# Performance work log

Measured on AMD Instinct MI355X. Metric: run time of the kernel, lower is better.

## Reference

```python
import jax, jax.numpy as jnp
import numpy as np

N_NODES = 50000
N_EDGES = 800000
IN_F = 128
OUT_F = 128
N_LAYERS = 2


def setup_inputs() -> dict:
    key = jax.random.key(0)
    ks = jax.random.split(key, 8)
    x = jax.random.normal(ks[0], (N_NODES, IN_F), dtype=jnp.float32)
    hidden_states = jax.random.normal(ks[1], (N_LAYERS, N_NODES, OUT_F), dtype=jnp.float32)
    src = jax.random.randint(ks[2], (N_EDGES,), 0, N_NODES)
    dst = jax.random.randint(ks[3], (N_EDGES,), 0, N_NODES)
    edge_w = jax.random.uniform(ks[4], (N_EDGES,), dtype=jnp.float32)
    # [layer, gate(r,u,c), in+out, out], scaled like typical init
    W_self = jax.random.normal(ks[5], (N_LAYERS, 3, IN_F + OUT_F, OUT_F), dtype=jnp.float32) * 0.05
    W_neigh = jax.random.normal(ks[6], (N_LAYERS, 3, IN_F + OUT_F, OUT_F), dtype=jnp.float32) * 0.05
    bias = jax.random.uniform(ks[7], (N_LAYERS, 3, OUT_F), dtype=jnp.float32)
    return {"x": x, "hidden_states": hidden_states, "src": src, "dst": dst,
            "edge_w": edge_w, "W_self": W_self, "W_neigh": W_neigh, "bias": bias}


def _gconv(z, src, dst, edge_w, ws, wn):
    # z: [N, 2F]; message passing: sum_{e: dst=v} edge_w[e] * z[src[e]]
    msg = z[src] * edge_w[:, None]                      # [E, 2F]
    agg = jax.ops.segment_sum(msg, dst, num_segments=N_NODES)  # [N, 2F]
    return z @ ws + agg @ wn                            # [N, F]


def _cell(x, h, src, dst, edge_w, ws, wn, b):
    # ws/wn: [3, 2F, F], b: [3, F]; gates r,u,c as in GraphGRUCell
    xh = jnp.concatenate([x, h], axis=1)
    r = jax.nn.sigmoid(_gconv(xh, src, dst, edge_w, ws[0], wn[0]) + b[0])
    u = jax.nn.sigmoid(_gconv(xh, src, dst, edge_w, ws[1], wn[1]) + b[1])
    xh2 = jnp.concatenate([x, r * h], axis=1)
    c = jax.nn.sigmoid(_gconv(xh2, src, dst, edge_w, ws[2], wn[2]) + b[2])
    return u * h + (1.0 - u) * c


def reference(x, hidden_states, src, dst, edge_w, W_self, W_neigh, bias):
    hiddens = []
    for i in range(N_LAYERS):  # small fixed layer count
        x = _cell(x, hidden_states[i], src, dst, edge_w, W_self[i], W_neigh[i], bias[i])
        hiddens.append(x)
    return (x, hiddens)
```

## Files before the change

kernel.cpp:

```cpp
#include <hip/hip_runtime.h>
#include <math.h>

#define F 128
#define NLAYERS 2

typedef __attribute__((ext_vector_type(8))) short bf16x8s;
typedef __attribute__((ext_vector_type(8))) unsigned short u16x8;
typedef __attribute__((ext_vector_type(4))) float f32x4;

__device__ __forceinline__ float sigmoidf_(float x) { return 1.0f / (1.0f + expf(-x)); }

__device__ __forceinline__ unsigned short f2bf(float f) {
    unsigned int u = __float_as_uint(f);
    u += 0x7fffu + ((u >> 16) & 1u);
    return (unsigned short)(u >> 16);
}
__device__ __forceinline__ float bf2f(unsigned short s) {
    return __uint_as_float(((unsigned int)s) << 16);
}

__global__ void pack_w_bf16(const float* __restrict__ Ws, const float* __restrict__ Wn,
                            unsigned short* __restrict__ W1b, unsigned short* __restrict__ W2b) {
    int t = blockIdx.x * blockDim.x + threadIdx.x;
    const int n1 = 2 * 64 * 256 * 8;
    if (t < n1) {
        int j = t & 7, n = (t >> 3) & 255, ko = (t >> 11) & 63, l = t >> 17;
        int k = ko * 8 + j;
        int p = k >> 7, r = k & 127, g = n >> 7, c = n & 127;
        const float* W = (p < 2) ? Ws : Wn;
        W1b[t] = f2bf(W[(((l * 3 + g) * 256) + ((p & 1) * 128 + r)) * 128 + c]);
    } else {
        int t2 = t - n1;
        if (t2 >= 2 * 64 * 128 * 8) return;
        int j = t2 & 7, n = (t2 >> 3) & 127, ko = (t2 >> 10) & 63, l = t2 >> 16;
        int k = ko * 8 + j;
        int p = k >> 7, r = k & 127;
        const float* W = (p < 2) ? Ws : Wn;
        W2b[t2] = f2bf(W[(((l * 3 + 2) * 256) + ((p & 1) * 128 + r)) * 128 + n]);
    }
}

__global__ void cvt_bf16_i(const float* __restrict__ in, unsigned short* __restrict__ out, int n4) {
    int t = blockIdx.x * blockDim.x + threadIdx.x;
    if (t >= n4) return;
    float4 v = reinterpret_cast<const float4*>(in)[t];
    ushort4 o;
    o.x = f2bf(v.x); o.y = f2bf(v.y); o.z = f2bf(v.z); o.w = f2bf(v.w);
    *reinterpret_cast<ushort4*>(out + (((size_t)(t >> 5)) << 8) + ((t & 31) << 2)) = o;
}

__global__ void hist_dst(const int* __restrict__ dst, int* __restrict__ cnt, int E) {
    int e = blockIdx.x * blockDim.x + threadIdx.x;
    if (e < E) atomicAdd(&cnt[dst[e]], 1);
}

__global__ __launch_bounds__(1024) void scan_blk(const int* __restrict__ cnt,
                                                 int* __restrict__ offs,
                                                 int* __restrict__ bsum, int n) {
    __shared__ int wsum[16];
    int tid = threadIdx.x, lane = tid & 63, wid = tid >> 6;
    int i = blockIdx.x * 1024 + tid;
    int v = (i < n) ? cnt[i] : 0;
    int incl = v;
#pragma unroll
    for (int off = 1; off < 64; off <<= 1) {
        int t = __shfl_up(incl, off, 64);
        if (lane >= off) incl += t;
    }
    if (lane == 63) wsum[wid] = incl;
    __syncthreads();
    if (wid == 0) {
        int s = (lane < 16) ? wsum[lane] : 0;
#pragma unroll
        for (int off = 1; off < 16; off <<= 1) {
            int t = __shfl_up(s, off, 64);
            if (lane >= off) s += t;
        }
        if (lane < 16) wsum[lane] = s;
    }
    __syncthreads();
    int wbase = (wid > 0) ? wsum[wid - 1] : 0;
    if (i < n) offs[i] = wbase + incl - v;
    if (tid == 1023) bsum[blockIdx.x] = wbase + incl;
}

__global__ __launch_bounds__(1024) void scan_tops(int* __restrict__ bsum, int nb,
                                                  int* __restrict__ total_out) {
    __shared__ int wsum[16];
    int tid = threadIdx.x, lane = tid & 63, wid = tid >> 6;
    int v = (tid < nb) ? bsum[tid] : 0;
    int incl = v;
#pragma unroll
    for (int off = 1; off < 64; off <<= 1) {
        int t = __shfl_up(incl, off, 64);
        if (lane >= off) incl += t;
    }
    if (lane == 63) wsum[wid] = incl;
    __syncthreads();
    if (wid == 0) {
        int s = (lane < 16) ? wsum[lane] : 0;
#pragma unroll
        for (int off = 1; off < 16; off <<= 1) {
            int t = __shfl_up(s, off, 64);
            if (lane >= off) s += t;
        }
        if (lane < 16) wsum[lane] = s;
    }
    __syncthreads();
    int wbase = (wid > 0) ? wsum[wid - 1] : 0;
    if (tid < nb) bsum[tid] = wbase + incl - v;
    if (tid == 1023) *total_out = wbase + incl;
}

__global__ __launch_bounds__(1024) void scan_add(const int* __restrict__ bsum,
                                                 int* __restrict__ offs,
                                                 int* __restrict__ cursor, int n) {
    int i = blockIdx.x * 1024 + threadIdx.x;
    if (i >= n) return;
    int o = offs[i] + bsum[blockIdx.x];
    offs[i] = o;
    cursor[i] = o;
}

__global__ void scatter_edges(const int* __restrict__ src, const int* __restrict__ dst,
                              const float* __restrict__ ew, int* __restrict__ cursor,
                              int2* __restrict__ es, int E) {
    int e = blockIdx.x * blockDim.x + threadIdx.x;
    if (e >= E) return;
    int d = dst[e];
    int p = atomicAdd(&cursor[d], 1);
    es[p] = make_int2(src[e], __float_as_int(ew[e]));
}

__global__ __launch_bounds__(256) void agg_csr2_i(
    const unsigned short* __restrict__ XH,
    const int2* __restrict__ es, const int* __restrict__ offs,
    unsigned short* __restrict__ agg0, unsigned short* __restrict__ agg1, int N) {
    int node = blockIdx.x * 8 + (threadIdx.x >> 5);
    if (node >= N) return;
    int lane = threadIdx.x & 31;
    int beg = offs[node], end = offs[node + 1];
    float a0[8] = {0, 0, 0, 0, 0, 0, 0, 0};
    float a1[8] = {0, 0, 0, 0, 0, 0, 0, 0};
    int loff = lane << 3;
    int i = beg;
    for (; i + 3 < end; i += 4) {
        int2 e0 = es[i], e1 = es[i + 1], e2 = es[i + 2], e3 = es[i + 3];
        u16x8 v0 = *reinterpret_cast<const u16x8*>(XH + (((size_t)e0.x) << 8) + loff);
        u16x8 v1 = *reinterpret_cast<const u16x8*>(XH + (((size_t)e1.x) << 8) + loff);
        u16x8 v2 = *reinterpret_cast<const u16x8*>(XH + (((size_t)e2.x) << 8) + loff);
        u16x8 v3 = *reinterpret_cast<const u16x8*>(XH + (((size_t)e3.x) << 8) + loff);
        float w0 = __int_as_float(e0.y), w1 = __int_as_float(e1.y);
        float w2 = __int_as_float(e2.y), w3 = __int_as_float(e3.y);
#pragma unroll
        for (int j = 0; j < 8; ++j) {
            a0[j] += w0 * bf2f(v0[j]);
            a1[j] += w1 * bf2f(v1[j]);
            a0[j] += w2 * bf2f(v2[j]);
            a1[j] += w3 * bf2f(v3[j]);
        }
    }
    for (; i < end; ++i) {
        int2 e0 = es[i];
        float w0 = __int_as_float(e0.y);
        u16x8 v0 = *reinterpret_cast<const u16x8*>(XH + (((size_t)e0.x) << 8) + loff);
#pragma unroll
        for (int j = 0; j < 8; ++j) a0[j] += w0 * bf2f(v0[j]);
    }
    u16x8 o;
#pragma unroll
    for (int j = 0; j < 8; ++j) o[j] = f2bf(a0[j] + a1[j]);
    unsigned short* op = (lane < 16)
        ? (agg0 + (((size_t)node) << 7) + (lane << 3))
        : (agg1 + (((size_t)node) << 7) + ((lane & 15) << 3));
    *reinterpret_cast<u16x8*>(op) = o;
}

__global__ __launch_bounds__(256) void agg_csr1_b(
    const unsigned short* __restrict__ V0,
    const int2* __restrict__ es, const int* __restrict__ offs,
    unsigned short* __restrict__ agg0, int N) {
    int node = blockIdx.x * 8 + (threadIdx.x >> 5);
    if (node >= N) return;
    int lane = threadIdx.x & 31;
    int beg = offs[node], end = offs[node + 1];
    float p0[4] = {0, 0, 0, 0}, p1[4] = {0, 0, 0, 0};
    int loff = lane << 2;
    int i = beg;
    for (; i + 3 < end; i += 4) {
        int2 e0 = es[i], e1 = es[i + 1], e2 = es[i + 2], e3 = es[i + 3];
        ushort4 x0 = *reinterpret_cast<const ushort4*>(V0 + (((size_t)e0.x) << 7) + loff);
        ushort4 x1 = *reinterpret_cast<const ushort4*>(V0 + (((size_t)e1.x) << 7) + loff);
        ushort4 x2 = *reinterpret_cast<const ushort4*>(V0 + (((size_t)e2.x) << 7) + loff);
        ushort4 x3 = *reinterpret_cast<const ushort4*>(V0 + (((size_t)e3.x) << 7) + loff);
        float w0 = __int_as_float(e0.y), w1 = __int_as_float(e1.y);
        float w2 = __int_as_float(e2.y), w3 = __int_as_float(e3.y);
        p0[0] += w0 * bf2f(x0.x); p0[1] += w0 * bf2f(x0.y);
        p0[2] += w0 * bf2f(x0.z); p0[3] += w0 * bf2f(x0.w);
        p1[0] += w1 * bf2f(x1.x); p1[1] += w1 * bf2f(x1.y);
        p1[2] += w1 * bf2f(x1.z); p1[3] += w1 * bf2f(x1.w);
        p0[0] += w2 * bf2f(x2.x); p0[1] += w2 * bf2f(x2.y);
        p0[2] += w2 * bf2f(x2.z); p0[3] += w2 * bf2f(x2.w);
        p1[0] += w3 * bf2f(x3.x); p1[1] += w3 * bf2f(x3.y);
        p1[2] += w3 * bf2f(x3.z); p1[3] += w3 * bf2f(x3.w);
    }
    for (; i < end; ++i) {
        int2 e0 = es[i];
        float w0 = __int_as_float(e0.y);
        ushort4 x0 = *reinterpret_cast<const ushort4*>(V0 + (((size_t)e0.x) << 7) + loff);
        p0[0] += w0 * bf2f(x0.x); p0[1] += w0 * bf2f(x0.y);
        p0[2] += w0 * bf2f(x0.z); p0[3] += w0 * bf2f(x0.w);
    }
    size_t ob = (((size_t)node) << 7) + loff;
    ushort4 o0;
    o0.x = f2bf(p0[0] + p1[0]); o0.y = f2bf(p0[1] + p1[1]);
    o0.z = f2bf(p0[2] + p1[2]); o0.w = f2bf(p0[3] + p1[3]);
    *reinterpret_cast<ushort4*>(agg0 + ob) = o0;
}

__global__ __launch_bounds__(256) void gemm_mfma(
    const unsigned short* __restrict__ A0, const unsigned short* __restrict__ A1,
    const unsigned short* __restrict__ A2, const unsigned short* __restrict__ A3,
    int sA0, int sA1, int obsh,
    const unsigned short* __restrict__ Wb, const float* __restrict__ bias,
    const float* __restrict__ hfull, const float* __restrict__ uin,
    unsigned short* __restrict__ outb, float* __restrict__ outf,
    float* __restrict__ outf2, int Nn, int Ntot, int mode) {
    __shared__ __align__(16) unsigned short Als[2][4 * 64 * 8];
    __shared__ __align__(16) unsigned short Bls[2][4 * 128 * 8];
    const unsigned short* parts[4] = {A0, A1, A2, A3};

    int tid = threadIdx.x;
    int row0 = blockIdx.x * 64;
    int n0c = blockIdx.y * 128;
    int lane = tid & 63;
    int w = tid >> 6;
    int wrow = (w & 1) << 5;
    int wcol = (w >> 1) << 6;
    int quad = lane >> 4, l16 = lane & 15;

    f32x4 acc[2][4];
    const f32x4 z4 = {0.f, 0.f, 0.f, 0.f};
#pragma unroll
    for (int mt = 0; mt < 2; ++mt)
#pragma unroll
        for (int nt = 0; nt < 4; ++nt) acc[mt][nt] = z4;

    int growA = row0 + lane;
    if (growA >= Nn) growA = Nn - 1;
    int qB = tid >> 7, nB = tid & 127;

    auto stage = [&](int ks, int buf) {
        int p = ks >> 7;
        size_t roff = (p == 0) ? (size_t)growA * (size_t)sA0
                    : (p == 1) ? (size_t)growA * (size_t)sA1
                               : ((size_t)growA << 7);
        const unsigned short* ga = parts[p] + roff + (ks & 127) + (w << 3);
        __builtin_amdgcn_global_load_lds(
            (const __attribute__((address_space(1))) void*)ga,
            (__attribute__((address_space(3))) void*)&Als[buf][((w << 6) + lane) << 3], 16, 0, 0);
#pragma unroll
        for (int r = 0; r < 2; ++r) {
            int q = 2 * r + qB;
            int koG = (ks >> 3) + q;
            const unsigned short* gb = Wb + ((size_t)(koG * Ntot + n0c + nB) << 3);
            __builtin_amdgcn_global_load_lds(
                (const __attribute__((address_space(1))) void*)gb,
                (__attribute__((address_space(3))) void*)&Bls[buf][((q << 7) + nB) << 3], 16, 0, 0);
        }
    };

    stage(0, 0);
    __syncthreads();
    int buf = 0;
    for (int ks = 0; ks < 512; ks += 32, buf ^= 1) {
        if (ks + 32 < 512) stage(ks + 32, buf ^ 1);

        bf16x8s af[2], bfr[4];
#pragma unroll
        for (int mt = 0; mt < 2; ++mt)
            af[mt] = *reinterpret_cast<const bf16x8s*>(
                &Als[buf][((quad << 6) + wrow + (mt << 4) + l16) << 3]);
#pragma unroll
        for (int nt = 0; nt < 4; ++nt)
            bfr[nt] = *reinterpret_cast<const bf16x8s*>(
                &Bls[buf][((quad << 7) + wcol + (nt << 4) + l16) << 3]);
#pragma unroll
        for (int mt = 0; mt < 2; ++mt)
#pragma unroll
            for (int nt = 0; nt < 4; ++nt)
                acc[mt][nt] = __builtin_amdgcn_mfma_f32_16x16x32_bf16(
                    af[mt], bfr[nt], acc[mt][nt], 0, 0, 0);
        __syncthreads();
    }

#pragma unroll
    for (int mt = 0; mt < 2; ++mt) {
#pragma unroll
        for (int reg = 0; reg < 4; ++reg) {
            int row = row0 + wrow + (mt << 4) + (quad << 2) + reg;
            if (row >= Nn) continue;
#pragma unroll
            for (int nt = 0; nt < 4; ++nt) {
                int col = n0c + wcol + (nt << 4) + l16;
                float val = acc[mt][nt][reg] + bias[col];
                if (mode == 0) {
                    float sg = sigmoidf_(val);
                    int c = col & 127;
                    size_t o = ((size_t)row << 7) + c;
                    if (col < 128)
                        outb[o] = f2bf(sg * hfull[o]);
                    else
                        outf[o] = sg;
                } else {
                    float cv = sigmoidf_(val);
                    size_t o = ((size_t)row << 7) + col;
                    float uu = uin[o];
                    float hh = hfull[o];
                    float hn = uu * hh + (1.0f - uu) * cv;
                    outf[o] = hn;
                    if (outf2) outf2[o] = hn;
                    outb[((size_t)row << obsh) + col] = f2bf(hn);
                }
            }
        }
    }
}

extern "C" void kernel_launch(void* const* d_in, const int* in_sizes, int n_in,
                              void* d_out, int out_size, void* d_ws, size_t ws_size,
                              hipStream_t stream) {
    const float* x      = (const float*)d_in[0];
    const float* hidden = (const float*)d_in[1];
    const int*   src    = (const int*)d_in[2];
    const int*   dst    = (const int*)d_in[3];
    const float* ew     = (const float*)d_in[4];
    const float* Wself  = (const float*)d_in[5];
    const float* Wneigh = (const float*)d_in[6];
    const float* bias   = (const float*)d_in[7];
    float* out = (float*)d_out;

    int N = in_sizes[0] / F;
    int E = in_sizes[2];
    size_t NF = (size_t)N * F;

    char* p = (char*)d_ws;
    auto alloc = [&](size_t bytes) { char* r = p; p += (bytes + 255) & ~255ull; return r; };
    unsigned short* xh0    = (unsigned short*)alloc(2 * NF * 2);
    unsigned short* xh1    = (unsigned short*)alloc(2 * NF * 2);
    unsigned short* agg_xb = (unsigned short*)alloc(NF * 2);
    unsigned short* agg_hb = (unsigned short*)alloc(NF * 2);
    unsigned short* agg_rb = (unsigned short*)alloc(NF * 2);
    unsigned short* rhb    = (unsigned short*)alloc(NF * 2);
    float*          u      = (float*)alloc(NF * 4);
    unsigned short* W1b    = (unsigned short*)alloc(2 * 64 * 256 * 8 * 2);
    unsigned short* W2b    = (unsigned short*)alloc(2 * 64 * 128 * 8 * 2);
    int2*           es     = (int2*)alloc((size_t)E * 8);
    int*            cnt    = (int*)alloc((size_t)N * 4);
    int*            offs   = (int*)alloc(((size_t)N + 1) * 4);
    int*            cursor = (int*)alloc((size_t)N * 4);
    int*            bsum   = (int*)alloc(1024 * 4);

    pack_w_bf16<<<dim3(1536), dim3(256), 0, stream>>>(Wself, Wneigh, W1b, W2b);
    int n4 = (int)(NF / 4);
    int cblk = (n4 + 255) / 256;
    cvt_bf16_i<<<dim3(cblk), dim3(256), 0, stream>>>(x, xh0, n4);
    cvt_bf16_i<<<dim3(cblk), dim3(256), 0, stream>>>(hidden, xh0 + 128, n4);
    cvt_bf16_i<<<dim3(cblk), dim3(256), 0, stream>>>(hidden + NF, xh1 + 128, n4);

    hipMemsetAsync(cnt, 0, (size_t)N * sizeof(int), stream);
    int eBlocks = (E + 255) / 256;
    hist_dst<<<dim3(eBlocks), dim3(256), 0, stream>>>(dst, cnt, E);
    int nb = (N + 1023) / 1024;
    scan_blk<<<dim3(nb), dim3(1024), 0, stream>>>(cnt, offs, bsum, N);
    scan_tops<<<dim3(1), dim3(1024), 0, stream>>>(bsum, nb, offs + N);
    scan_add<<<dim3(nb), dim3(1024), 0, stream>>>(bsum, offs, cursor, N);
    scatter_edges<<<dim3(eBlocks), dim3(256), 0, stream>>>(src, dst, ew, cursor, es, E);

    float* out_x  = out;
    float* out_h1 = out + NF;
    float* out_h2 = out + 2 * NF;

    int aggBlocks = (N + 7) / 8;
    int mBlocks = (N + 63) / 64;
    for (int l = 0; l < NLAYERS; ++l) {
        unsigned short* xhL = (l == 0) ? xh0 : xh1;
        const float* hL = hidden + (size_t)l * NF;
        const float* biasL = bias + (size_t)l * 384;

        agg_csr2_i<<<dim3(aggBlocks), dim3(256), 0, stream>>>(xhL, es, offs,
                                                              agg_xb, agg_hb, N);

        gemm_mfma<<<dim3(mBlocks, 2), dim3(256), 0, stream>>>(
            xhL, xhL + 128, agg_xb, agg_hb, 256, 256, 7,
            W1b + (size_t)l * 64 * 256 * 8, biasL, hL, nullptr,
            rhb, u, nullptr, N, 256, 0);

        agg_csr1_b<<<dim3(aggBlocks), dim3(256), 0, stream>>>(rhb, es, offs, agg_rb, N);

        float* o1 = (l == 0) ? out_h1 : out_h2;
        float* o2 = (l == NLAYERS - 1) ? out_x : nullptr;
        unsigned short* obN = (l == 0) ? xh1 : agg_rb;
        int obsh = (l == 0) ? 8 : 7;
        gemm_mfma<<<dim3(mBlocks, 1), dim3(256), 0, stream>>>(
            xhL, rhb, agg_xb, agg_rb, 256, 128, obsh,
            W2b + (size_t)l * 64 * 128 * 8, biasL + 256, hL, u,
            obN, o1, o2, N, 128, 1);
    }
}
```

Baseline: 608.5 us.

## Fuse neighbor aggregation into MFMA gate GEMMs and merge conversion kernels

Fuses the CSR gather-aggregation into the r/u and c GEMM kernels, so the aggregated tile lives in swizzled shared memory instead of being written to and re-read from global memory. The r/u GEMM now covers all 256 output columns in one block instead of splitting across two blocks. The three bf16 conversion launches are merged into one. In exchange, each fused block runs a serial gather phase before its GEMM, with large LDS use that may lower occupancy and limit overlap of gather latency with MFMA work.

New measurement: 715.1 us. 17.5% more time.

```diff
diff --git a/kernel.cpp b/kernel.cpp
--- a/kernel.cpp
+++ b/kernel.cpp
@@ -40,13 +40,21 @@
     }
 }
 
-__global__ void cvt_bf16_i(const float* __restrict__ in, unsigned short* __restrict__ out, int n4) {
+__global__ void cvt_all(const float* __restrict__ x, const float* __restrict__ hidden,
+                        unsigned short* __restrict__ xh0, unsigned short* __restrict__ xh1,
+                        int n4, size_t NF) {
     int t = blockIdx.x * blockDim.x + threadIdx.x;
-    if (t >= n4) return;
-    float4 v = reinterpret_cast<const float4*>(in)[t];
+    const float* in;
+    unsigned short* out;
+    int tt;
+    if (t < n4) { in = x; out = xh0; tt = t; }
+    else if (t < 2 * n4) { in = hidden; out = xh0 + 128; tt = t - n4; }
+    else if (t < 3 * n4) { in = hidden + NF; out = xh1 + 128; tt = t - 2 * n4; }
+    else return;
+    float4 v = reinterpret_cast<const float4*>(in)[tt];
     ushort4 o;
     o.x = f2bf(v.x); o.y = f2bf(v.y); o.z = f2bf(v.z); o.w = f2bf(v.w);
-    *reinterpret_cast<ushort4*>(out + (((size_t)(t >> 5)) << 8) + ((t & 31) << 2)) = o;
+    *reinterpret_cast<ushort4*>(out + (((size_t)(tt >> 5)) << 8) + ((tt & 31) << 2)) = o;
 }
 
 __global__ void hist_dst(const int* __restrict__ dst, int* __restrict__ cnt, int E) {
@@ -132,112 +140,245 @@
     es[p] = make_int2(src[e], __float_as_int(ew[e]));
 }
 
-__global__ __launch_bounds__(256) void agg_csr2_i(
+__global__ __launch_bounds__(256) void fused_ru(
     const unsigned short* __restrict__ XH,
     const int2* __restrict__ es, const int* __restrict__ offs,
-    unsigned short* __restrict__ agg0, unsigned short* __restrict__ agg1, int N) {
-    int node = blockIdx.x * 8 + (threadIdx.x >> 5);
-    if (node >= N) return;
-    int lane = threadIdx.x & 31;
-    int beg = offs[node], end = offs[node + 1];
-    float a0[8] = {0, 0, 0, 0, 0, 0, 0, 0};
-    float a1[8] = {0, 0, 0, 0, 0, 0, 0, 0};
-    int loff = lane << 3;
-    int i = beg;
-    for (; i + 3 < end; i += 4) {
-        int2 e0 = es[i], e1 = es[i + 1], e2 = es[i + 2], e3 = es[i + 3];
-        u16x8 v0 = *reinterpret_cast<const u16x8*>(XH + (((size_t)e0.x) << 8) + loff);
-        u16x8 v1 = *reinterpret_cast<const u16x8*>(XH + (((size_t)e1.x) << 8) + loff);
-        u16x8 v2 = *reinterpret_cast<const u16x8*>(XH + (((size_t)e2.x) << 8) + loff);
-        u16x8 v3 = *reinterpret_cast<const u16x8*>(XH + (((size_t)e3.x) << 8) + loff);
-        float w0 = __int_as_float(e0.y), w1 = __int_as_float(e1.y);
-        float w2 = __int_as_float(e2.y), w3 = __int_as_float(e3.y);
-#pragma unroll
-        for (int j = 0; j < 8; ++j) {
-            a0[j] += w0 * bf2f(v0[j]);
-            a1[j] += w1 * bf2f(v1[j]);
-            a0[j] += w2 * bf2f(v2[j]);
-            a1[j] += w3 * bf2f(v3[j]);
-        }
-    }
-    for (; i < end; ++i) {
-        int2 e0 = es[i];
-        float w0 = __int_as_float(e0.y);
-        u16x8 v0 = *reinterpret_cast<const u16x8*>(XH + (((size_t)e0.x) << 8) + loff);
-#pragma unroll
-        for (int j = 0; j < 8; ++j) a0[j] += w0 * bf2f(v0[j]);
-    }
-    u16x8 o;
-#pragma unroll
-    for (int j = 0; j < 8; ++j) o[j] = f2bf(a0[j] + a1[j]);
-    unsigned short* op = (lane < 16)
-        ? (agg0 + (((size_t)node) << 7) + (lane << 3))
-        : (agg1 + (((size_t)node) << 7) + ((lane & 15) << 3));
-    *reinterpret_cast<u16x8*>(op) = o;
-}
-
-__global__ __launch_bounds__(256) void agg_csr1_b(
-    const unsigned short* __restrict__ V0,
+    const unsigned short* __restrict__ Wb, const float* __restrict__ bias,
+    const float* __restrict__ hfull,
+    unsigned short* __restrict__ aggx_out,
+    unsigned short* __restrict__ rhb, float* __restrict__ u, int N) {
+    __shared__ __align__(16) unsigned short AGG[64 * 256];
+    __shared__ __align__(16) unsigned short Als[2][4 * 64 * 8];
+    __shared__ __align__(16) unsigned short Bls[2][4 * 256 * 8];
+
+    int tid = threadIdx.x;
+    int row0 = blockIdx.x * 64;
+    int lane64 = tid & 63, w = tid >> 6;
+    int lane32 = tid & 31, grp = tid >> 5;
+
+    int growA = row0 + lane64;
+    if (growA >= N) growA = N - 1;
+
+    {
+        const unsigned short* ga = XH + (size_t)growA * 256 + (w << 3);
+        __builtin_amdgcn_global_load_lds(
+            (const __attribute__((address_space(1))) void*)ga,
+            (__attribute__((address_space(3))) void*)&Als[0][((w << 6) + lane64) << 3], 16, 0, 0);
+#pragma unroll
+        for (int r = 0; r < 4; ++r) {
+            int idx = (r << 8) + tid;
+            int q = idx >> 8, n = idx & 255;
+            const unsigned short* gb = Wb + ((size_t)(q * 256 + n) << 3);
+            __builtin_amdgcn_global_load_lds(
+                (const __attribute__((address_space(1))) void*)gb,
+                (__attribute__((address_space(3))) void*)&Bls[0][((q << 8) + n) << 3], 16, 0, 0);
+        }
+    }
+
+    int loff = lane32 << 3;
+    for (int ln = grp; ln < 64; ln += 8) {
+        int node = row0 + ln;
+        float a0[8] = {0, 0, 0, 0, 0, 0, 0, 0};
+        float a1[8] = {0, 0, 0, 0, 0, 0, 0, 0};
+        if (node < N) {
+            int beg = offs[node], end = offs[node + 1];
+            int i = beg;
+            for (; i + 3 < end; i += 4) {
+                int2 e0 = es[i], e1 = es[i + 1], e2 = es[i + 2], e3 = es[i + 3];
+                u16x8 v0 = *reinterpret_cast<const u16x8*>(XH + (((size_t)e0.x) << 8) + loff);
+                u16x8 v1 = *reinterpret_cast<const u16x8*>(XH + (((size_t)e1.x) << 8) + loff);
+                u16x8 v2 = *reinterpret_cast<const u16x8*>(XH + (((size_t)e2.x) << 8) + loff);
+                u16x8 v3 = *reinterpret_cast<const u16x8*>(XH + (((size_t)e3.x) << 8) + loff);
+                float w0 = __int_as_float(e0.y), w1 = __int_as_float(e1.y);
+                float w2 = __int_as_float(e2.y), w3 = __int_as_float(e3.y);
+#pragma unroll
+                for (int j = 0; j < 8; ++j) {
+                    a0[j] += w0 * bf2f(v0[j]);
+                    a1[j] += w1 * bf2f(v1[j]);
+                    a0[j] += w2 * bf2f(v2[j]);
+                    a1[j] += w3 * bf2f(v3[j]);
+                }
+            }
+            for (; i < end; ++i) {
+                int2 e0 = es[i];
+                float w0 = __int_as_float(e0.y);
+                u16x8 v0 = *reinterpret_cast<const u16x8*>(XH + (((size_t)e0.x) << 8) + loff);
+#pragma unroll
+                for (int j = 0; j < 8; ++j) a0[j] += w0 * bf2f(v0[j]);
+            }
+        }
+        u16x8 o;
+#pragma unroll
+        for (int j = 0; j < 8; ++j) o[j] = f2bf(a0[j] + a1[j]);
+        int sidx = ln * 256 + ((lane32 << 3) ^ ((ln & 7) << 3));
+        *reinterpret_cast<u16x8*>(&AGG[sidx]) = o;
+        if (node < N && lane32 < 16)
+            *reinterpret_cast<u16x8*>(aggx_out + (((size_t)node) << 7) + (lane32 << 3)) = o;
+    }
+    __syncthreads();
+
+    int wrow = (w & 1) << 5;
+    int wcol = (w >> 1) << 7;
+    int quad = lane64 >> 4, l16 = lane64 & 15;
+
+    f32x4 acc[2][8];
+    const f32x4 z4 = {0.f, 0.f, 0.f, 0.f};
+#pragma unroll
+    for (int mt = 0; mt < 2; ++mt)
+#pragma unroll
+        for (int nt = 0; nt < 8; ++nt) acc[mt][nt] = z4;
+
+    int buf = 0;
+    for (int ks = 0; ks < 512; ks += 32, buf ^= 1) {
+        int nk = ks + 32;
+        if (nk < 512) {
+#pragma unroll
+            for (int r = 0; r < 4; ++r) {
+                int idx = (r << 8) + tid;
+                int q = idx >> 8, n = idx & 255;
+                int koG = (nk >> 3) + q;
+                const unsigned short* gb = Wb + ((size_t)(koG * 256 + n) << 3);
+                __builtin_amdgcn_global_load_lds(
+                    (const __attribute__((address_space(1))) void*)gb,
+                    (__attribute__((address_space(3))) void*)&Bls[buf ^ 1][((q << 8) + n) << 3], 16, 0, 0);
+            }
+            if (nk < 256) {
+                const unsigned short* ga = XH + (size_t)growA * 256 + nk + (w << 3);
+                __builtin_amdgcn_global_load_lds(
+                    (const __attribute__((address_space(1))) void*)ga,
+                    (__attribute__((address_space(3))) void*)&Als[buf ^ 1][((w << 6) + lane64) << 3], 16, 0, 0);
+            }
+        }
+
+        bf16x8s af[2], bfr[8];
+        if (ks < 256) {
+#pragma unroll
+            for (int mt = 0; mt < 2; ++mt)
+                af[mt] = *reinterpret_cast<const bf16x8s*>(
+                    &Als[buf][((quad << 6) + wrow + (mt << 4) + l16) << 3]);
+        } else {
+            int colk = (ks - 256) + (quad << 3);
+#pragma unroll
+            for (int mt = 0; mt < 2; ++mt) {
+                int row = wrow + (mt << 4) + l16;
+                af[mt] = *reinterpret_cast<const bf16x8s*>(
+                    &AGG[row * 256 + (colk ^ ((row & 7) << 3))]);
+            }
+        }
+#pragma unroll
+        for (int nt = 0; nt < 8; ++nt)
+            bfr[nt] = *reinterpret_cast<const bf16x8s*>(
+                &Bls[buf][((quad << 8) + wcol + (nt << 4) + l16) << 3]);
+#pragma unroll
+        for (int mt = 0; mt < 2; ++mt)
+#pragma unroll
+            for (int nt = 0; nt < 8; ++nt)
+                acc[mt][nt] = __builtin_amdgcn_mfma_f32_16x16x32_bf16(
+                    af[mt], bfr[nt], acc[mt][nt], 0, 0, 0);
+        __syncthreads();
+    }
+
+#pragma unroll
+    for (int mt = 0; mt < 2; ++mt) {
+#pragma unroll
+        for (int reg = 0; reg < 4; ++reg) {
+            int row = row0 + wrow + (mt << 4) + (quad << 2) + reg;
+            if (row >= N) continue;
+#pragma unroll
+            for (int nt = 0; nt < 8; ++nt) {
+                int col = wcol + (nt << 4) + l16;
+                float val = acc[mt][nt][reg] + bias[col];
+                float sg = sigmoidf_(val);
+                int c = col & 127;
+                size_t o = ((size_t)row << 7) + c;
+                if (col < 128)
+                    rhb[o] = f2bf(sg * hfull[o]);
+                else
+                    u[o] = sg;
+            }
+        }
+    }
+}
+
+__global__ __launch_bounds__(256) void fused_c(
+    const unsigned short* __restrict__ XH, const unsigned short* __restrict__ RHB,
+    const unsigned short* __restrict__ AGGX,
     const int2* __restrict__ es, const int* __restrict__ offs,
-    unsigned short* __restrict__ agg0, int N) {
-    int node = blockIdx.x * 8 + (threadIdx.x >> 5);
-    if (node >= N) return;
-    int lane = threadIdx.x & 31;
-    int beg = offs[node], end = offs[node + 1];
-    float p0[4] = {0, 0, 0, 0}, p1[4] = {0, 0, 0, 0};
-    int loff = lane << 2;
-    int i = beg;
-    for (; i + 3 < end; i += 4) {
-        int2 e0 = es[i], e1 = es[i + 1], e2 = es[i + 2], e3 = es[i + 3];
-        ushort4 x0 = *reinterpret_cast<const ushort4*>(V0 + (((size_t)e0.x) << 7) + loff);
-        ushort4 x1 = *reinterpret_cast<const ushort4*>(V0 + (((size_t)e1.x) << 7) + loff);
-        ushort4 x2 = *reinterpret_cast<const ushort4*>(V0 + (((size_t)e2.x) << 7) + loff);
-        ushort4 x3 = *reinterpret_cast<const ushort4*>(V0 + (((size_t)e3.x) << 7) + loff);
-        float w0 = __int_as_float(e0.y), w1 = __int_as_float(e1.y);
-        float w2 = __int_as_float(e2.y), w3 = __int_as_float(e3.y);
-        p0[0] += w0 * bf2f(x0.x); p0[1] += w0 * bf2f(x0.y);
-        p0[2] += w0 * bf2f(x0.z); p0[3] += w0 * bf2f(x0.w);
-        p1[0] += w1 * bf2f(x1.x); p1[1] += w1 * bf2f(x1.y);
-        p1[2] += w1 * bf2f(x1.z); p1[3] += w1 * bf2f(x1.w);
-        p0[0] += w2 * bf2f(x2.x); p0[1] += w2 * bf2f(x2.y);
-        p0[2] += w2 * bf2f(x2.z); p0[3] += w2 * bf2f(x2.w);
-        p1[0] += w3 * bf2f(x3.x); p1[1] += w3 * bf2f(x3.y);
-        p1[2] += w3 * bf2f(x3.z); p1[3] += w3 * bf2f(x3.w);
-    }
-    for (; i < end; ++i) {
-        int2 e0 = es[i];
-        float w0 = __int_as_float(e0.y);
-        ushort4 x0 = *reinterpret_cast<const ushort4*>(V0 + (((size_t)e0.x) << 7) + loff);
-        p0[0] += w0 * bf2f(x0.x); p0[1] += w0 * bf2f(x0.y);
-        p0[2] += w0 * bf2f(x0.z); p0[3] += w0 * bf2f(x0.w);
-    }
-    size_t ob = (((size_t)node) << 7) + loff;
-    ushort4 o0;
-    o0.x = f2bf(p0[0] + p1[0]); o0.y = f2bf(p0[1] + p1[1]);
-    o0.z = f2bf(p0[2] + p1[2]); o0.w = f2bf(p0[3] + p1[3]);
-    *reinterpret_cast<ushort4*>(agg0 + ob) = o0;
-}
-
-__global__ __launch_bounds__(256) void gemm_mfma(
-    const unsigned short* __restrict__ A0, const unsigned short* __restrict__ A1,
-    const unsigned short* __restrict__ A2, const unsigned short* __restrict__ A3,
-    int sA0, int sA1, int obsh,
     const unsigned short* __restrict__ Wb, const float* __restrict__ bias,
     const float* __restrict__ hfull, const float* __restrict__ uin,
     unsigned short* __restrict__ outb, float* __restrict__ outf,
-    float* __restrict__ outf2, int Nn, int Ntot, int mode) {
+    float* __restrict__ outf2, int obsh, int N) {
+    __shared__ __align__(16) unsigned short AGG[64 * 128];
     __shared__ __align__(16) unsigned short Als[2][4 * 64 * 8];
     __shared__ __align__(16) unsigned short Bls[2][4 * 128 * 8];
-    const unsigned short* parts[4] = {A0, A1, A2, A3};
 
     int tid = threadIdx.x;
     int row0 = blockIdx.x * 64;
-    int n0c = blockIdx.y * 128;
-    int lane = tid & 63;
-    int w = tid >> 6;
+    int lane64 = tid & 63, w = tid >> 6;
+    int lane32 = tid & 31, grp = tid >> 5;
+
+    int growA = row0 + lane64;
+    if (growA >= N) growA = N - 1;
+
+    {
+        const unsigned short* ga = XH + (size_t)growA * 256 + (w << 3);
+        __builtin_amdgcn_global_load_lds(
+            (const __attribute__((address_space(1))) void*)ga,
+            (__attribute__((address_space(3))) void*)&Als[0][((w << 6) + lane64) << 3], 16, 0, 0);
+#pragma unroll
+        for (int r = 0; r < 2; ++r) {
+            int idx = (r << 8) + tid;
+            int q = idx >> 7, n = idx & 127;
+            const unsigned short* gb = Wb + ((size_t)(q * 128 + n) << 3);
+            __builtin_amdgcn_global_load_lds(
+                (const __attribute__((address_space(1))) void*)gb,
+                (__attribute__((address_space(3))) void*)&Bls[0][((q << 7) + n) << 3], 16, 0, 0);
+        }
+    }
+
+    int loff = lane32 << 2;
+    for (int ln = grp; ln < 64; ln += 8) {
+        int node = row0 + ln;
+        float p0[4] = {0, 0, 0, 0}, p1[4] = {0, 0, 0, 0};
+        if (node < N) {
+            int beg = offs[node], end = offs[node + 1];
+            int i = beg;
+            for (; i + 3 < end; i += 4) {
+                int2 e0 = es[i], e1 = es[i + 1], e2 = es[i + 2], e3 = es[i + 3];
+                ushort4 x0 = *reinterpret_cast<const ushort4*>(RHB + (((size_t)e0.x) << 7) + loff);
+                ushort4 x1 = *reinterpret_cast<const ushort4*>(RHB + (((size_t)e1.x) << 7) + loff);
+                ushort4 x2 = *reinterpret_cast<const ushort4*>(RHB + (((size_t)e2.x) << 7) + loff);
+                ushort4 x3 = *reinterpret_cast<const ushort4*>(RHB + (((size_t)e3.x) << 7) + loff);
+                float w0 = __int_as_float(e0.y), w1 = __int_as_float(e1.y);
+                float w2 = __int_as_float(e2.y), w3 = __int_as_float(e3.y);
+                p0[0] += w0 * bf2f(x0.x); p0[1] += w0 * bf2f(x0.y);
+                p0[2] += w0 * bf2f(x0.z); p0[3] += w0 * bf2f(x0.w);
+                p1[0] += w1 * bf2f(x1.x); p1[1] += w1 * bf2f(x1.y);
+                p1[2] += w1 * bf2f(x1.z); p1[3] += w1 * bf2f(x1.w);
+                p0[0] += w2 * bf2f(x2.x); p0[1] += w2 * bf2f(x2.y);
+                p0[2] += w2 * bf2f(x2.z); p0[3] += w2 * bf2f(x2.w);
+                p1[0] += w3 * bf2f(x3.x); p1[1] += w3 * bf2f(x3.y);
+                p1[2] += w3 * bf2f(x3.z); p1[3] += w3 * bf2f(x3.w);
+            }
+            for (; i < end; ++i) {
+                int2 e0 = es[i];
+                float w0 = __int_as_float(e0.y);
+                ushort4 x0 = *reinterpret_cast<const ushort4*>(RHB + (((size_t)e0.x) << 7) + loff);
+                p0[0] += w0 * bf2f(x0.x); p0[1] += w0 * bf2f(x0.y);
+                p0[2] += w0 * bf2f(x0.z); p0[3] += w0 * bf2f(x0.w);
+            }
+        }
+        ushort4 o;
+        o.x = f2bf(p0[0] + p1[0]); o.y = f2bf(p0[1] + p1[1]);
+        o.z = f2bf(p0[2] + p1[2]); o.w = f2bf(p0[3] + p1[3]);
+        int sidx = ln * 128 + ((lane32 << 2) ^ ((ln & 7) << 3));
+        *reinterpret_cast<ushort4*>(&AGG[sidx]) = o;
+    }
+    __syncthreads();
+
     int wrow = (w & 1) << 5;
     int wcol = (w >> 1) << 6;
-    int quad = lane >> 4, l16 = lane & 15;
+    int quad = lane64 >> 4, l16 = lane64 & 15;
 
     f32x4 acc[2][4];
     const f32x4 z4 = {0.f, 0.f, 0.f, 0.f};
@@ -246,41 +387,47 @@
 #pragma unroll
         for (int nt = 0; nt < 4; ++nt) acc[mt][nt] = z4;
 
-    int growA = row0 + lane;
-    if (growA >= Nn) growA = Nn - 1;
-    int qB = tid >> 7, nB = tid & 127;
-
-    auto stage = [&](int ks, int buf) {
-        int p = ks >> 7;
-        size_t roff = (p == 0) ? (size_t)growA * (size_t)sA0
-                    : (p == 1) ? (size_t)growA * (size_t)sA1
-                               : ((size_t)growA << 7);
-        const unsigned short* ga = parts[p] + roff + (ks & 127) + (w << 3);
-        __builtin_amdgcn_global_load_lds(
-            (const __attribute__((address_space(1))) void*)ga,
-            (__attribute__((address_space(3))) void*)&Als[buf][((w << 6) + lane) << 3], 16, 0, 0);
-#pragma unroll
-        for (int r = 0; r < 2; ++r) {
-            int q = 2 * r + qB;
-            int koG = (ks >> 3) + q;
-            const unsigned short* gb = Wb + ((size_t)(koG * Ntot + n0c + nB) << 3);
-            __builtin_amdgcn_global_load_lds(
-                (const __attribute__((address_space(1))) void*)gb,
-                (__attribute__((address_space(3))) void*)&Bls[buf][((q << 7) + nB) << 3], 16, 0, 0);
-        }
-    };
-
-    stage(0, 0);
-    __syncthreads();
     int buf = 0;
     for (int ks = 0; ks < 512; ks += 32, buf ^= 1) {
-        if (ks + 32 < 512) stage(ks + 32, buf ^ 1);
+        int nk = ks + 32;
+        if (nk < 512) {
+#pragma unroll
+            for (int r = 0; r < 2; ++r) {
+                int idx = (r << 8) + tid;
+                int q = idx >> 7, n = idx & 127;
+                int koG = (nk >> 3) + q;
+                const unsigned short* gb = Wb + ((size_t)(koG * 128 + n) << 3);
+                __builtin_amdgcn_global_load_lds(
+                    (const __attribute__((address_space(1))) void*)gb,
+                    (__attribute__((address_space(3))) void*)&Bls[buf ^ 1][((q << 7) + n) << 3], 16, 0, 0);
+            }
+            if (nk < 384) {
+                int p = nk >> 7;
+                const unsigned short* ga =
+                    (p == 0) ? (XH + (size_t)growA * 256 + (nk & 127) + (w << 3))
+                  : (p == 1) ? (RHB + (size_t)growA * 128 + (nk & 127) + (w << 3))
+                             : (AGGX + (size_t)growA * 128 + (nk & 127) + (w << 3));
+                __builtin_amdgcn_global_load_lds(
+                    (const __attribute__((address_space(1))) void*)ga,
+                    (__attribute__((address_space(3))) void*)&Als[buf ^ 1][((w << 6) + lane64) << 3], 16, 0, 0);
+            }
+        }
 
         bf16x8s af[2], bfr[4];
-#pragma unroll
-        for (int mt = 0; mt < 2; ++mt)
-            af[mt] = *reinterpret_cast<const bf16x8s*>(
-                &Als[buf][((quad << 6) + wrow + (mt << 4) + l16) << 3]);
+        if (ks < 384) {
+#pragma unroll
+            for (int mt = 0; mt < 2; ++mt)
+                af[mt] = *reinterpret_cast<const bf16x8s*>(
+                    &Als[buf][((quad << 6) + wrow + (mt << 4) + l16) << 3]);
+        } else {
+            int colk = (ks - 384) + (quad << 3);
+#pragma unroll
+            for (int mt = 0; mt < 2; ++mt) {
+                int row = wrow + (mt << 4) + l16;
+                af[mt] = *reinterpret_cast<const bf16x8s*>(
+                    &AGG[row * 128 + (colk ^ ((row & 7) << 3))]);
+            }
+        }
 #pragma unroll
         for (int nt = 0; nt < 4; ++nt)
             bfr[nt] = *reinterpret_cast<const bf16x8s*>(
@@ -299,29 +446,19 @@
 #pragma unroll
         for (int reg = 0; reg < 4; ++reg) {
             int row = row0 + wrow + (mt << 4) + (quad << 2) + reg;
-            if (row >= Nn) continue;
+            if (row >= N) continue;
 #pragma unroll
             for (int nt = 0; nt < 4; ++nt) {
-                int col = n0c + wcol + (nt << 4) + l16;
+                int col = wcol + (nt << 4) + l16;
                 float val = acc[mt][nt][reg] + bias[col];
-                if (mode == 0) {
-                    float sg = sigmoidf_(val);
-                    int c = col & 127;
-                    size_t o = ((size_t)row << 7) + c;
-                    if (col < 128)
-                        outb[o] = f2bf(sg * hfull[o]);
-                    else
-                        outf[o] = sg;
-                } else {
-                    float cv = sigmoidf_(val);
-                    size_t o = ((size_t)row << 7) + col;
-                    float uu = uin[o];
-                    float hh = hfull[o];
-                    float hn = uu * hh + (1.0f - uu) * cv;
-                    outf[o] = hn;
-                    if (outf2) outf2[o] = hn;
-                    outb[((size_t)row << obsh) + col] = f2bf(hn);
-                }
+                float cv = sigmoidf_(val);
+                size_t o = ((size_t)row << 7) + col;
+                float uu = uin[o];
+                float hh = hfull[o];
+                float hn = uu * hh + (1.0f - uu) * cv;
+                outf[o] = hn;
+                if (outf2) outf2[o] = hn;
+                outb[((size_t)row << obsh) + col] = f2bf(hn);
             }
         }
     }
@@ -349,8 +486,6 @@
     unsigned short* xh0    = (unsigned short*)alloc(2 * NF * 2);
     unsigned short* xh1    = (unsigned short*)alloc(2 * NF * 2);
     unsigned short* agg_xb = (unsigned short*)alloc(NF * 2);
-    unsigned short* agg_hb = (unsigned short*)alloc(NF * 2);
-    unsigned short* agg_rb = (unsigned short*)alloc(NF * 2);
     unsigned short* rhb    = (unsigned short*)alloc(NF * 2);
     float*          u      = (float*)alloc(NF * 4);
     unsigned short* W1b    = (unsigned short*)alloc(2 * 64 * 256 * 8 * 2);
@@ -363,10 +498,7 @@
 
     pack_w_bf16<<<dim3(1536), dim3(256), 0, stream>>>(Wself, Wneigh, W1b, W2b);
     int n4 = (int)(NF / 4);
-    int cblk = (n4 + 255) / 256;
-    cvt_bf16_i<<<dim3(cblk), dim3(256), 0, stream>>>(x, xh0, n4);
-    cvt_bf16_i<<<dim3(cblk), dim3(256), 0, stream>>>(hidden, xh0 + 128, n4);
-    cvt_bf16_i<<<dim3(cblk), dim3(256), 0, stream>>>(hidden + NF, xh1 + 128, n4);
+    cvt_all<<<dim3((3 * n4 + 255) / 256), dim3(256), 0, stream>>>(x, hidden, xh0, xh1, n4, NF);
 
     hipMemsetAsync(cnt, 0, (size_t)N * sizeof(int), stream);
     int eBlocks = (E + 255) / 256;
@@ -381,30 +513,23 @@
     float* out_h1 = out + NF;
     float* out_h2 = out + 2 * NF;
 
-    int aggBlocks = (N + 7) / 8;
     int mBlocks = (N + 63) / 64;
     for (int l = 0; l < NLAYERS; ++l) {
         unsigned short* xhL = (l == 0) ? xh0 : xh1;
         const float* hL = hidden + (size_t)l * NF;
         const float* biasL = bias + (size_t)l * 384;
 
-        agg_csr2_i<<<dim3(aggBlocks), dim3(256), 0, stream>>>(xhL, es, offs,
-                                                              agg_xb, agg_hb, N);
-
-        gemm_mfma<<<dim3(mBlocks, 2), dim3(256), 0, stream>>>(
-            xhL, xhL + 128, agg_xb, agg_hb, 256, 256, 7,
-            W1b + (size_t)l * 64 * 256 * 8, biasL, hL, nullptr,
-            rhb, u, nullptr, N, 256, 0);
-
-        agg_csr1_b<<<dim3(aggBlocks), dim3(256), 0, stream>>>(rhb, es, offs, agg_rb, N);
+        fused_ru<<<dim3(mBlocks), dim3(256), 0, stream>>>(
+            xhL, es, offs, W1b + (size_t)l * 64 * 256 * 8, biasL, hL,
+            agg_xb, rhb, u, N);
 
         float* o1 = (l == 0) ? out_h1 : out_h2;
         float* o2 = (l == NLAYERS - 1) ? out_x : nullptr;
-        unsigned short* obN = (l == 0) ? xh1 : agg_rb;
+        unsigned short* obN = (l == 0) ? xh1 : agg_xb;
         int obsh = (l == 0) ? 8 : 7;
-        gemm_mfma<<<dim3(mBlocks, 1), dim3(256), 0, stream>>>(
-            xhL, rhb, agg_xb, agg_rb, 256, 128, obsh,
+        fused_c<<<dim3(mBlocks), dim3(256), 0, stream>>>(
+            xhL, rhb, agg_xb, es, offs,
             W2b + (size_t)l * 64 * 128 * 8, biasL + 256, hL, u,
-            obN, o1, o2, N, 128, 1);
-    }
-}
+            obN, o1, o2, obsh, N);
+    }
+}
```
